# Optimization experiments

Hardware: AMD Instinct MI355X
Metric: run time of the kernel (lower is better)

The kernel has to match this reference:

```python
import jax, jax.numpy as jnp
import numpy as np
import math

IN_FEATURES = 512
KERNEL = 3
EPS = 1e-08
GAIN = 1.0 / math.sqrt(IN_FEATURES * KERNEL * KERNEL)  # lr_multiplier=1


def setup_inputs() -> dict:
    key = jax.random.key(0)
    k1, k2, k3 = jax.random.split(key, 3)
    x = jax.random.normal(k1, (16, 512, 32, 32), dtype=jnp.float32)
    style = jax.random.normal(k2, (16, 512), dtype=jnp.float32)
    weight = jax.random.normal(k3, (512, 512, 3, 3), dtype=jnp.float32)
    return {"x": x, "style": style, "weight": weight}


def reference(x, style, weight):
    # w: [B, O, I, k, k] = gain-scaled weight modulated per-sample by style over input channels
    w = (weight * GAIN)[None] * style[:, None, :, None, None]
    # demodulate: rsqrt of sum of squares over (I, kh, kw) per (B, O)
    sigma = jax.lax.rsqrt(jnp.sum(jnp.square(w), axis=(2, 3, 4)) + EPS)
    w = w * sigma[:, :, None, None, None]
    # per-sample conv2d with padding='same' (stride 1, k=3 -> pad 1)
    def conv_one(xi, wi):  # xi: [C,H,W], wi: [O,I,k,k]
        return jax.lax.conv_general_dilated(
            xi[None], wi, window_strides=(1, 1), padding='SAME',
            dimension_numbers=('NCHW', 'OIHW', 'NCHW'))[0]
    return jax.vmap(conv_one)(x, w)  # [B, O, H, W]
```

## Files before the change

### kernel.cpp

```cpp
#include <hip/hip_runtime.h>
#include <hip/hip_bf16.h>

#define EPSF 1e-8f
#define GAINF 0.014731391274719739f

typedef __attribute__((ext_vector_type(8))) __bf16 bf16x8;
typedef __attribute__((ext_vector_type(4))) __bf16 bf16x4;
typedef __attribute__((ext_vector_type(16))) float f32x16;

#define GLOAD_LDS16(gp, lp) __builtin_amdgcn_global_load_lds( \
    (const __attribute__((address_space(1))) unsigned int*)(gp), \
    (__attribute__((address_space(3))) unsigned int*)(lp), 16, 0, 0)

__global__ void k_prep(const float* __restrict__ x, const float* __restrict__ style,
                       const float* __restrict__ w, float* __restrict__ S,
                       __hip_bfloat16* __restrict__ wbf, __hip_bfloat16* __restrict__ xs) {
  int blk = blockIdx.x, tid = threadIdx.x;
  if (blk < 2048) {
    __shared__ float tile[64][65];
    int b = blk >> 7, rem = blk & 127, ct = rem >> 4, pt = rem & 15;
    int p0 = pt * 64, c0 = ct * 64;
    int tx = tid & 63, ty = tid >> 6;
#pragma unroll
    for (int k = 0; k < 16; ++k) {
      int ci = ty + k * 4;
      tile[ci][tx] = x[((b * 512) + (c0 + ci)) * 1024 + p0 + tx];
    }
    __syncthreads();
    int tq = tid & 15, py = tid >> 4;
    int c = c0 + tq * 4;
    int cb = c >> 5, cw = c & 31;
    float st0 = style[b * 512 + c], st1 = style[b * 512 + c + 1];
    float st2 = style[b * 512 + c + 2], st3 = style[b * 512 + c + 3];
#pragma unroll
    for (int k = 0; k < 4; ++k) {
      int pl = py + k * 16;
      int p = p0 + pl;
      int y = p >> 5, xx = p & 31;
      int site = (y + 1) * 34 + (xx + 1);
      bf16x4 v;
      v[0] = (__bf16)(tile[tq * 4 + 0][pl] * st0);
      v[1] = (__bf16)(tile[tq * 4 + 1][pl] * st1);
      v[2] = (__bf16)(tile[tq * 4 + 2][pl] * st2);
      v[3] = (__bf16)(tile[tq * 4 + 3][pl] * st3);
      *reinterpret_cast<bf16x4*>(xs + (size_t)(((b * 16 + cb) * 1156 + site) * 32 + cw)) = v;
    }
  } else if (blk < 3072) {
    int idx = (blk - 2048) * 256 + tid;
    int o = idx >> 9, i = idx & 511;
    const float* p = w + (size_t)idx * 9;
    float s = 0.f;
#pragma unroll
    for (int t = 0; t < 9; ++t) {
      float v = p[t];
      s += v * v;
      wbf[(size_t)t * 262144 + (i >> 5) * 16384 + o * 32 + (i & 31)] = __float2bfloat16(v);
    }
    S[idx] = s;
  } else {
    int bb = blk - 3072;
    int b = bb >> 4, cb = bb & 15;
    for (int i2 = tid; i2 < 528; i2 += 256) {
      int sb = i2 >> 2, q = i2 & 3;
      int yp, xp;
      if (sb < 34) { yp = 0; xp = sb; }
      else if (sb < 68) { yp = 33; xp = sb - 34; }
      else { int t2 = sb - 68; yp = 1 + (t2 >> 1); xp = (t2 & 1) * 33; }
      float4 z = {0.f, 0.f, 0.f, 0.f};
      *reinterpret_cast<float4*>(xs + (size_t)(((b * 16 + cb) * 1156 + yp * 34 + xp) * 32 + q * 8)) = z;
    }
  }
}

__global__ void k_sigma(const float* __restrict__ style, const float* __restrict__ S,
                        float* __restrict__ esc) {
  __shared__ float s2[8192];
  __shared__ float red[4][16];
  int tid = threadIdx.x, o = blockIdx.x;
  for (int idx = tid; idx < 8192; idx += 256) {
    float v = style[idx];
    s2[idx] = v * v;
  }
  __syncthreads();
  float acc[16];
#pragma unroll
  for (int b = 0; b < 16; ++b) acc[b] = 0.f;
  for (int i = tid; i < 512; i += 256) {
    float s = S[o * 512 + i];
#pragma unroll
    for (int b = 0; b < 16; ++b) acc[b] += s2[b * 512 + i] * s;
  }
#pragma unroll
  for (int b = 0; b < 16; ++b)
#pragma unroll
    for (int off = 32; off; off >>= 1) acc[b] += __shfl_down(acc[b], off);
  int lane = tid & 63, wv = tid >> 6;
  if (lane == 0)
#pragma unroll
    for (int b = 0; b < 16; ++b) red[wv][b] = acc[b];
  __syncthreads();
  if (tid < 16) {
    float s = red[0][tid] + red[1][tid] + red[2][tid] + red[3][tid];
    esc[tid * 512 + o] = GAINF * rsqrtf(s * (GAINF * GAINF) + EPSF);
  }
}

__global__ __launch_bounds__(64, 1) void k_conv(
    const __hip_bfloat16* __restrict__ wbf, const __hip_bfloat16* __restrict__ xs,
    const float* __restrict__ esc, float* __restrict__ out) {
  __shared__ __hip_bfloat16 ldsB[2 * 6528];
  int g = blockIdx.x;
  int xcd = g & 7, sblk = g >> 3;
  int m = sblk >> 4;
  int n = xcd * 16 + (sblk & 15);
  int b = n >> 3, nt = n & 7;
  int row0 = nt * 4;
  int lane = threadIdx.x;
  int l31 = lane & 31, lhi = lane >> 5;

  int roff[13];
#pragma unroll
  for (int j = 0; j < 13; ++j) {
    int idx = lane + j * 64;
    int site = idx >> 2, q0 = idx & 3;
    int qs = q0 ^ ((site >> 1) & 3);
    roff[j] = site * 32 + qs * 8;
  }

#define STAGE(cbv) do { \
    const __hip_bfloat16* _g = xs + (size_t)((b * 16 + (cbv)) * 1156 + row0 * 34) * 32; \
    __hip_bfloat16* _l = ldsB + ((cbv) & 1) * 6528 + lane * 8; \
    _Pragma("unroll") \
    for (int _j = 0; _j < 12; ++_j) GLOAD_LDS16(_g + roff[_j], _l + _j * 512); \
    if (lane < 48) GLOAD_LDS16(_g + roff[12], _l + 12 * 512); \
  } while (0)

  int wrow = (m * 64 + l31) * 32 + lhi * 8;
#define LOADA(dst, t_, cb_) do { \
    const __hip_bfloat16* _p = wbf + (size_t)(t_) * 262144 + (cb_) * 16384 + wrow; \
    dst[0][0] = *reinterpret_cast<const bf16x8*>(_p); \
    dst[0][1] = *reinterpret_cast<const bf16x8*>(_p + 1024); \
    dst[1][0] = *reinterpret_cast<const bf16x8*>(_p + 16); \
    dst[1][1] = *reinterpret_cast<const bf16x8*>(_p + 1024 + 16); \
  } while (0)

  f32x16 acc[2][4];
#pragma unroll
  for (int i = 0; i < 2; ++i)
#pragma unroll
    for (int j = 0; j < 4; ++j)
#pragma unroll
      for (int e = 0; e < 16; ++e) acc[i][j][e] = 0.f;

  bf16x8 aC[2][2], aN[2][2];
  STAGE(0);
  LOADA(aC, 0, 0);

  for (int cb = 0; cb < 16; ++cb) {
    __syncthreads();
    if (cb < 15) STAGE(cb + 1);
    const __hip_bfloat16* lb = ldsB + (cb & 1) * 6528;
#pragma unroll
    for (int t = 0; t < 9; ++t) {
      const int dy = t / 3, dx = t - dy * 3;
      if (cb < 15 || t < 8) {
        int tn = (t == 8) ? 0 : t + 1;
        int cbn = (t == 8) ? cb + 1 : cb;
        LOADA(aN, tn, cbn);
      }
      int s[4], sw[4];
#pragma unroll
      for (int ns = 0; ns < 4; ++ns) {
        s[ns] = (ns + dy) * 34 + l31 + dx;
        sw[ns] = (s[ns] >> 1) & 3;
      }
#pragma unroll
      for (int k2 = 0; k2 < 2; ++k2) {
        int ko = (k2 << 1) | lhi;
        bf16x8 bf[4];
#pragma unroll
        for (int ns = 0; ns < 4; ++ns)
          bf[ns] = *reinterpret_cast<const bf16x8*>(&lb[(s[ns] * 4 + (ko ^ sw[ns])) * 8]);
#pragma unroll
        for (int ns = 0; ns < 4; ++ns) {
          acc[0][ns] = __builtin_amdgcn_mfma_f32_32x32x16_bf16(aC[k2][0], bf[ns], acc[0][ns], 0, 0, 0);
          acc[1][ns] = __builtin_amdgcn_mfma_f32_32x32x16_bf16(aC[k2][1], bf[ns], acc[1][ns], 0, 0, 0);
        }
      }
#pragma unroll
      for (int k2 = 0; k2 < 2; ++k2)
#pragma unroll
        for (int ms = 0; ms < 2; ++ms)
          aC[k2][ms] = aN[k2][ms];
    }
  }
  int pxb = nt * 128 + l31;
#pragma unroll
  for (int ms = 0; ms < 2; ++ms)
#pragma unroll
    for (int reg = 0; reg < 16; ++reg) {
      int o = m * 64 + ms * 32 + (reg & 3) + ((reg >> 2) << 3) + (lhi << 2);
      float e = esc[(b << 9) + o];
#pragma unroll
      for (int ns = 0; ns < 4; ++ns)
        out[(size_t)((b << 9) + o) * 1024 + pxb + ns * 32] = acc[ms][ns][reg] * e;
    }
#undef STAGE
#undef LOADA
}

extern "C" void kernel_launch(void* const* d_in, const int* in_sizes, int n_in,
                              void* d_out, int out_size, void* d_ws, size_t ws_size,
                              hipStream_t stream) {
  const float* x = (const float*)d_in[0];
  const float* style = (const float*)d_in[1];
  const float* w = (const float*)d_in[2];
  float* out = (float*)d_out;
  char* ws = (char*)d_ws;
  __hip_bfloat16* wbf = (__hip_bfloat16*)(ws);
  __hip_bfloat16* xs  = (__hip_bfloat16*)(ws + 4718592);
  float* S   = (float*)(ws + 23658496);
  float* esc = (float*)(ws + 24707072);

  hipLaunchKernelGGL(k_prep, dim3(3328), dim3(256), 0, stream, x, style, w, S, wbf, xs);
  hipLaunchKernelGGL(k_sigma, dim3(512), dim3(256), 0, stream, style, S, esc);
  hipLaunchKernelGGL(k_conv, dim3(1024), dim3(64), 0, stream, wbf, xs, esc, out);
}
```

Baseline: 174.6 us.

## Share staged input tile across four waves per block in conv kernel

Restructures the conv kernel from single-wave blocks computing 64 output channels to 256-thread blocks where four waves each compute 32 channels and cooperatively stage a shared input tile in LDS. This cuts redundant global-to-LDS staging of the activation tile and lowers per-wave register use, allowing more waves per CU. In exchange each LDS B-fragment read now feeds half as many MFMAs, raising the LDS-read to compute ratio.

```diff
diff --git a/kernel.cpp b/kernel.cpp
--- a/kernel.cpp
+++ b/kernel.cpp
@@ -105,23 +105,25 @@
   }
 }
 
-__global__ __launch_bounds__(64, 1) void k_conv(
+__global__ __launch_bounds__(256, 2) void k_conv(
     const __hip_bfloat16* __restrict__ wbf, const __hip_bfloat16* __restrict__ xs,
     const float* __restrict__ esc, float* __restrict__ out) {
   __shared__ __hip_bfloat16 ldsB[2 * 6528];
   int g = blockIdx.x;
   int xcd = g & 7, sblk = g >> 3;
-  int m = sblk >> 4;
+  int mg = sblk >> 4;
   int n = xcd * 16 + (sblk & 15);
   int b = n >> 3, nt = n & 7;
   int row0 = nt * 4;
-  int lane = threadIdx.x;
+  int tid = threadIdx.x;
+  int wv = tid >> 6, lane = tid & 63;
   int l31 = lane & 31, lhi = lane >> 5;
-
-  int roff[13];
-#pragma unroll
-  for (int j = 0; j < 13; ++j) {
-    int idx = lane + j * 64;
+  int o_base = mg * 128 + wv * 32;
+
+  int roff[4];
+#pragma unroll
+  for (int j = 0; j < 4; ++j) {
+    int idx = wv * 204 + j * 64 + lane;
     int site = idx >> 2, q0 = idx & 3;
     int qs = q0 ^ ((site >> 1) & 3);
     roff[j] = site * 32 + qs * 8;
@@ -129,30 +131,26 @@
 
 #define STAGE(cbv) do { \
     const __hip_bfloat16* _g = xs + (size_t)((b * 16 + (cbv)) * 1156 + row0 * 34) * 32; \
-    __hip_bfloat16* _l = ldsB + ((cbv) & 1) * 6528 + lane * 8; \
+    __hip_bfloat16* _l = ldsB + ((cbv) & 1) * 6528 + wv * 1632 + lane * 8; \
     _Pragma("unroll") \
-    for (int _j = 0; _j < 12; ++_j) GLOAD_LDS16(_g + roff[_j], _l + _j * 512); \
-    if (lane < 48) GLOAD_LDS16(_g + roff[12], _l + 12 * 512); \
+    for (int _j = 0; _j < 3; ++_j) GLOAD_LDS16(_g + roff[_j], _l + _j * 512); \
+    if (lane < 12) GLOAD_LDS16(_g + roff[3], _l + 3 * 512); \
   } while (0)
 
-  int wrow = (m * 64 + l31) * 32 + lhi * 8;
+  int wrow = (o_base + l31) * 32 + lhi * 8;
 #define LOADA(dst, t_, cb_) do { \
     const __hip_bfloat16* _p = wbf + (size_t)(t_) * 262144 + (cb_) * 16384 + wrow; \
-    dst[0][0] = *reinterpret_cast<const bf16x8*>(_p); \
-    dst[0][1] = *reinterpret_cast<const bf16x8*>(_p + 1024); \
-    dst[1][0] = *reinterpret_cast<const bf16x8*>(_p + 16); \
-    dst[1][1] = *reinterpret_cast<const bf16x8*>(_p + 1024 + 16); \
+    dst[0] = *reinterpret_cast<const bf16x8*>(_p); \
+    dst[1] = *reinterpret_cast<const bf16x8*>(_p + 16); \
   } while (0)
 
-  f32x16 acc[2][4];
-#pragma unroll
-  for (int i = 0; i < 2; ++i)
-#pragma unroll
-    for (int j = 0; j < 4; ++j)
-#pragma unroll
-      for (int e = 0; e < 16; ++e) acc[i][j][e] = 0.f;
-
-  bf16x8 aC[2][2], aN[2][2];
+  f32x16 acc[4];
+#pragma unroll
+  for (int j = 0; j < 4; ++j)
+#pragma unroll
+    for (int e = 0; e < 16; ++e) acc[j][e] = 0.f;
+
+  bf16x8 aC[2], aN[2];
   STAGE(0);
   LOADA(aC, 0, 0);
 
@@ -182,29 +180,22 @@
         for (int ns = 0; ns < 4; ++ns)
           bf[ns] = *reinterpret_cast<const bf16x8*>(&lb[(s[ns] * 4 + (ko ^ sw[ns])) * 8]);
 #pragma unroll
-        for (int ns = 0; ns < 4; ++ns) {
-          acc[0][ns] = __builtin_amdgcn_mfma_f32_32x32x16_bf16(aC[k2][0], bf[ns], acc[0][ns], 0, 0, 0);
-          acc[1][ns] = __builtin_amdgcn_mfma_f32_32x32x16_bf16(aC[k2][1], bf[ns], acc[1][ns], 0, 0, 0);
-        }
+        for (int ns = 0; ns < 4; ++ns)
+          acc[ns] = __builtin_amdgcn_mfma_f32_32x32x16_bf16(aC[k2], bf[ns], acc[ns], 0, 0, 0);
       }
-#pragma unroll
-      for (int k2 = 0; k2 < 2; ++k2)
-#pragma unroll
-        for (int ms = 0; ms < 2; ++ms)
-          aC[k2][ms] = aN[k2][ms];
+      aC[0] = aN[0];
+      aC[1] = aN[1];
     }
   }
   int pxb = nt * 128 + l31;
 #pragma unroll
-  for (int ms = 0; ms < 2; ++ms)
-#pragma unroll
-    for (int reg = 0; reg < 16; ++reg) {
-      int o = m * 64 + ms * 32 + (reg & 3) + ((reg >> 2) << 3) + (lhi << 2);
-      float e = esc[(b << 9) + o];
-#pragma unroll
-      for (int ns = 0; ns < 4; ++ns)
-        out[(size_t)((b << 9) + o) * 1024 + pxb + ns * 32] = acc[ms][ns][reg] * e;
-    }
+  for (int reg = 0; reg < 16; ++reg) {
+    int o = o_base + (reg & 3) + ((reg >> 2) << 3) + (lhi << 2);
+    float e = esc[(b << 9) + o];
+#pragma unroll
+    for (int ns = 0; ns < 4; ++ns)
+      out[(size_t)((b << 9) + o) * 1024 + pxb + ns * 32] = acc[ns][reg] * e;
+  }
 #undef STAGE
 #undef LOADA
 }
@@ -224,5 +215,5 @@
 
   hipLaunchKernelGGL(k_prep, dim3(3328), dim3(256), 0, stream, x, style, w, S, wbf, xs);
   hipLaunchKernelGGL(k_sigma, dim3(512), dim3(256), 0, stream, style, S, esc);
-  hipLaunchKernelGGL(k_conv, dim3(1024), dim3(64), 0, stream, wbf, xs, esc, out);
-}
+  hipLaunchKernelGGL(k_conv, dim3(512), dim3(256), 0, stream, wbf, xs, esc, out);
+}
```

Result: faster. 166.0 us (-4.9%).
